# Kernel tuning notes

Measured on AMD Instinct MI355X. Metric: run time of the kernel, lower is better.

## Reference

```python
import jax, jax.numpy as jnp
import numpy as np

N = 50000
E = 800000
IN_DIM = 128
HID = 32
HEADS = 8
OUT_DIM = 2
NEG_SLOPE = 0.2


def setup_inputs() -> dict:
    key = jax.random.key(0)
    ks = jax.random.split(key, 10)
    x = jax.random.normal(ks[0], (N, IN_DIM), dtype=jnp.float32)
    edge_index = jax.random.randint(ks[1], (2, E), 0, N, dtype=jnp.int64)
    s = 0.1
    W1 = jax.random.normal(ks[2], (IN_DIM, HEADS * HID), dtype=jnp.float32) * s
    att_src1 = jax.random.normal(ks[3], (HEADS, HID), dtype=jnp.float32) * s
    att_dst1 = jax.random.normal(ks[4], (HEADS, HID), dtype=jnp.float32) * s
    b1 = jnp.zeros((HEADS * HID,), dtype=jnp.float32)
    W2 = jax.random.normal(ks[5], (HEADS * HID, OUT_DIM), dtype=jnp.float32) * s
    att_src2 = jax.random.normal(ks[6], (1, OUT_DIM), dtype=jnp.float32) * s
    att_dst2 = jax.random.normal(ks[7], (1, OUT_DIM), dtype=jnp.float32) * s
    b2 = jnp.zeros((OUT_DIM,), dtype=jnp.float32)
    return {"x": x, "edge_index": edge_index, "W1": W1, "att_src1": att_src1,
            "att_dst1": att_dst1, "b1": b1, "W2": W2, "att_src2": att_src2,
            "att_dst2": att_dst2, "b2": b2}


def gat_conv(x, src, dst, W, att_src, att_dst, bias, concat):
    # PyG GATConv (add_self_loops handled by caller already appended in src/dst)
    H, C = att_src.shape
    n = x.shape[0]
    h = (x @ W).reshape(n, H, C)                       # [N,H,C]
    a_src = jnp.einsum('nhc,hc->nh', h, att_src)       # [N,H]
    a_dst = jnp.einsum('nhc,hc->nh', h, att_dst)       # [N,H]
    e = jax.nn.leaky_relu(a_src[src] + a_dst[dst], NEG_SLOPE)  # [Etot,H]
    m = jax.lax.stop_gradient(jax.ops.segment_max(e, dst, num_segments=n))
    ee = jnp.exp(e - m[dst])
    denom = jax.ops.segment_sum(ee, dst, num_segments=n)
    alpha = ee / denom[dst]                            # segment softmax over incoming edges
    out = jax.ops.segment_sum(alpha[:, :, None] * h[src], dst, num_segments=n)  # [N,H,C]
    if concat:
        out = out.reshape(n, H * C)
    else:
        out = out.mean(axis=1)
    return out + bias


def reference(x, edge_index, W1, att_src1, att_dst1, b1, W2, att_src2, att_dst2, b2):
    n = x.shape[0]
    loop = jnp.arange(n, dtype=edge_index.dtype)
    src = jnp.concatenate([edge_index[0], loop])
    dst = jnp.concatenate([edge_index[1], loop])
    h = gat_conv(x, src, dst, W1, att_src1, att_dst1, b1, concat=True)
    h = jax.nn.elu(h)
    # dropout inactive in eval mode
    h = gat_conv(h, src, dst, W2, att_src2, att_dst2, b2, concat=False)
    return jax.nn.log_softmax(h, axis=1)
```

## Files before the change

kernel.cpp:

```cpp
#include <hip/hip_runtime.h>
#include <hip/hip_bf16.h>

#define NEG_SLOPE 0.2f
#define BSTRIDE 6144

typedef float f32x4 __attribute__((ext_vector_type(4)));
typedef short s16x4 __attribute__((ext_vector_type(4)));
typedef short bf16x8 __attribute__((ext_vector_type(8)));

__device__ __forceinline__ float lrelu(float x) { return x > 0.f ? x : NEG_SLOPE * x; }
__device__ __forceinline__ float bf2f(unsigned u) {
    return __uint_as_float(u << 16);
}
__device__ __forceinline__ unsigned short f2bf(float f) {
    unsigned int u = __float_as_uint(f);
    return (unsigned short)((u + 0x7FFF + ((u >> 16) & 1)) >> 16);
}

__global__ __launch_bounds__(256) void prep_kernel(
        const float* __restrict__ W1, const float* __restrict__ att_src1,
        const float* __restrict__ att_dst1, unsigned short* __restrict__ w1t,
        const int* __restrict__ ei, int* __restrict__ flag, int* __restrict__ bktCur) {
    int t = threadIdx.x;
    if (blockIdx.x < 128) {
        int v = blockIdx.x * 256 + t;
        int col = v & 255, k = v >> 8;
        w1t[(size_t)col * 128 + k] = f2bf(W1[(size_t)k * 256 + col]);
    } else if (blockIdx.x == 128) {
#pragma unroll
        for (int i = 0; i < 8; ++i) {
            int v = t + 256 * i;
            int j = v & 15, k = v >> 4;
            const float* av = (j < 8) ? att_src1 : att_dst1;
            int h = j & 7;
            float s = 0.f;
            for (int c = 0; c < 32; ++c)
                s += W1[(size_t)k * 256 + 32 * h + c] * av[h * 32 + c];
            w1t[(size_t)(256 + j) * 128 + k] = f2bf(s);
        }
    } else {
        bktCur[t] = t * BSTRIDE;
        if (t == 0) {
            int z = 1;
            for (int k = 0; k < 64; ++k) if (ei[2 * k + 1] != 0) { z = 0; break; }
            *flag = z;
        }
    }
}

__global__ __launch_bounds__(256) void bin_scatter(const int* __restrict__ ei, int E, int n,
                                                   const int* __restrict__ flag,
                                                   int* __restrict__ bktCur,
                                                   int* __restrict__ binned) {
    __shared__ int hist[256];
    __shared__ int gb[256];
    int t = threadIdx.x;
    hist[t] = 0;
    __syncthreads();
    int is64 = *flag;
    int base = blockIdx.x * 2048;
    int Etot = E + n;
    int rec[8], rb[8], rr[8];
#pragma unroll
    for (int k = 0; k < 8; ++k) {
        int e = base + k * 256 + t;
        rb[k] = -1;
        if (e < Etot) {
            int s, d;
            if (e < E) {
                if (is64) {
                    s = ((const int2*)ei)[e].x;
                    d = ((const int2*)(ei + 2 * (size_t)E))[e].x;
                } else {
                    s = ei[e];
                    d = ei[(size_t)E + e];
                }
            } else { s = d = e - E; }
            int b = d >> 8;
            rb[k] = b;
            rec[k] = s | ((d & 255) << 24);
            rr[k] = atomicAdd(&hist[b], 1);
        }
    }
    __syncthreads();
    if (hist[t]) gb[t] = atomicAdd(&bktCur[t], hist[t]);
    __syncthreads();
#pragma unroll
    for (int k = 0; k < 8; ++k)
        if (rb[k] >= 0) binned[gb[rb[k]] + rr[k]] = rec[k];
}

__device__ __forceinline__ bf16x8 read_frag(const char* base, int row, int kb) {
    int swz = (row & 7) << 4;
    const char* p = base + row * 256;
    s16x4 lo = *(const s16x4*)(p + (kb ^ swz));
    s16x4 hi = *(const s16x4*)(p + ((kb + 32) ^ swz));
    return __builtin_shufflevector(lo, hi, 0, 1, 2, 3, 4, 5, 6, 7);
}

__device__ __forceinline__ void load_px(const float* __restrict__ x, int m0, int n, int t,
                                        f32x4 (&px)[2][4]) {
#pragma unroll
    for (int q = 0; q < 2; ++q) {
        int u = t + 256 * q;
        int row = u >> 3, kseg = u & 7;
        int gr = m0 + row;
        bool ok = (u < 384) && (gr < n);
        const f32x4* p = (const f32x4*)(x + (size_t)gr * 128 + kseg * 16);
#pragma unroll
        for (int j = 0; j < 4; ++j) {
            f32x4 z = {0.f, 0.f, 0.f, 0.f};
            px[q][j] = ok ? p[j] : z;
        }
    }
}

#define XOFF 69632
__global__ __launch_bounds__(256, 2) void build_gemm_kernel(
        const int* __restrict__ bktCur, const int* __restrict__ binned,
        int* __restrict__ offs, int* __restrict__ degOut, int* __restrict__ csr,
        const float* __restrict__ x, const unsigned short* __restrict__ w1t,
        unsigned short* __restrict__ h1u, float* __restrict__ asrc1,
        float* __restrict__ adst1, int n, int nchunk, int ngemm) {
    __shared__ __align__(16) char lds[81920];
    const int t = threadIdx.x;

    if (blockIdx.x >= ngemm) {
        int* deg = (int*)lds;
        int* sd  = (int*)(lds + 1024);
        int b = blockIdx.x - ngemm;
        int lo = b * BSTRIDE, hi = bktCur[b];
        deg[t] = 0;
        __syncthreads();
        for (int i = lo + t; i < hi; i += 256)
            atomicAdd(&deg[((unsigned)binned[i]) >> 24], 1);
        __syncthreads();
        int v = deg[t];
        sd[t] = v;
        __syncthreads();
        for (int o = 1; o < 256; o <<= 1) {
            int xv = (t >= o) ? sd[t - o] : 0;
            __syncthreads();
            sd[t] += xv;
            __syncthreads();
        }
        int excl = lo + sd[t] - v;
        int node = (b << 8) + t;
        if (node < n) { offs[node] = excl; degOut[node] = v; }
        __syncthreads();
        deg[t] = excl;
        __syncthreads();
        for (int i = lo + t; i < hi; i += 256) {
            unsigned r = (unsigned)binned[i];
            int pos = atomicAdd(&deg[r >> 24], 1);
            csr[pos] = (int)(r & 0xFFFFFF);
        }
        return;
    }

    const int lane = t & 63, w = t >> 6;
    const int l15 = lane & 15, g = lane >> 4;

    for (int u = t; u < 4352; u += 256) {
        int col = u >> 4, seg = u & 15;
        int4 v = *(const int4*)(w1t + (size_t)col * 128 + seg * 8);
        *(int4*)(lds + col * 256 + ((seg * 16) ^ ((col & 7) << 4))) = v;
    }

    int c0 = blockIdx.x * 2;
    f32x4 px[2][4];
    load_px(x, c0 * 48, n, t, px);
    __syncthreads();

    bf16x8 Bf[4][5];
#pragma unroll
    for (int ks = 0; ks < 4; ++ks) {
#pragma unroll
        for (int nt = 0; nt < 5; ++nt) {
            if (nt < 4 || w == 0) {
                int col = (nt < 4) ? (64 * w + 16 * nt + l15) : (256 + l15);
                Bf[ks][nt] = read_frag(lds, col, 64 * ks + 8 * g);
            }
        }
    }

    for (int cc = 0; cc < 2; ++cc) {
        int chunk = c0 + cc;
        if (chunk >= nchunk) break;
        int m0 = chunk * 48;
#pragma unroll
        for (int q = 0; q < 2; ++q) {
            int u = t + 256 * q;
            if (u < 384) {
                int row = u >> 3, kseg = u & 7;
                union { unsigned short us[16]; int4 v[2]; } pk;
#pragma unroll
                for (int j = 0; j < 4; ++j)
#pragma unroll
                    for (int e = 0; e < 4; ++e) pk.us[j * 4 + e] = f2bf(px[q][j][e]);
                int base = XOFF + row * 256;
                int swz = (row & 7) << 4;
                *(int4*)(lds + base + ((kseg * 32) ^ swz)) = pk.v[0];
                *(int4*)(lds + base + ((kseg * 32 + 16) ^ swz)) = pk.v[1];
            }
        }
        __syncthreads();
        if (cc == 0) load_px(x, (c0 + 1) * 48, n, t, px);

        f32x4 acc[3][5];
#pragma unroll
        for (int mt = 0; mt < 3; ++mt)
#pragma unroll
            for (int nt = 0; nt < 5; ++nt)
#pragma unroll
                for (int r = 0; r < 4; ++r) acc[mt][nt][r] = 0.f;

#pragma unroll
        for (int ks = 0; ks < 4; ++ks) {
            bf16x8 Af[3];
#pragma unroll
            for (int mt = 0; mt < 3; ++mt)
                Af[mt] = read_frag(lds + XOFF, mt * 16 + l15, 64 * ks + 8 * g);
#pragma unroll
            for (int nt = 0; nt < 5; ++nt) {
                if (nt < 4 || w == 0) {
#pragma unroll
                    for (int mt = 0; mt < 3; ++mt)
                        acc[mt][nt] = __builtin_amdgcn_mfma_f32_16x16x32_bf16(
                            Af[mt], Bf[ks][nt], acc[mt][nt], 0, 0, 0);
                }
            }
        }

#pragma unroll
        for (int mt = 0; mt < 3; ++mt) {
#pragma unroll
            for (int r = 0; r < 4; ++r) {
                int row = m0 + 16 * mt + 4 * g + r;
                bool ok = row < n;
#pragma unroll
                for (int nt = 0; nt < 4; ++nt)
                    if (ok) h1u[(size_t)row * 256 + 64 * w + 16 * nt + l15] =
                        f2bf(acc[mt][nt][r]);
                if (w == 0 && ok) {
                    float v = acc[mt][4][r];
                    if (l15 < 8) asrc1[(size_t)row * 8 + l15] = v;
                    else         adst1[(size_t)row * 8 + (l15 - 8)] = v;
                }
            }
        }
        if (cc == 0) __syncthreads();
    }
}

__global__ __launch_bounds__(64) void aggregate_kernel(
        const int* __restrict__ offs, const int* __restrict__ deg,
        const int* __restrict__ csr,
        const float* __restrict__ asrc1, const float* __restrict__ adst1,
        const unsigned short* __restrict__ h1u, const float* __restrict__ b1,
        const float* __restrict__ W2, const float* __restrict__ att_src2,
        const float* __restrict__ att_dst2, float4* __restrict__ rec) {
    int d = blockIdx.x;
    int t = threadIdx.x;
    int h = t >> 3;
    int off = offs[d], end = off + deg[d];
    float ad = adst1[(size_t)d * 8 + h];
    float a0 = 0.f, a1 = 0.f, a2 = 0.f, a3 = 0.f, aw = 0.f;
    const unsigned short* hp = h1u + 4 * t;
    int i = off;
    for (; i + 8 <= end; i += 8) {
        int sIdx[8];
#pragma unroll
        for (int k = 0; k < 8; ++k) sIdx[k] = csr[i + k];
        float wv[8];
#pragma unroll
        for (int k = 0; k < 8; ++k)
            wv[k] = __expf(lrelu(asrc1[(size_t)sIdx[k] * 8 + h] + ad));
        ushort4 hv[8];
#pragma unroll
        for (int k = 0; k < 8; ++k)
            hv[k] = *(const ushort4*)(hp + (size_t)sIdx[k] * 256);
#pragma unroll
        for (int k = 0; k < 8; ++k) {
            a0 = fmaf(wv[k], bf2f(hv[k].x), a0);
            a1 = fmaf(wv[k], bf2f(hv[k].y), a1);
            a2 = fmaf(wv[k], bf2f(hv[k].z), a2);
            a3 = fmaf(wv[k], bf2f(hv[k].w), a3);
            aw += wv[k];
        }
    }
    for (; i < end; ++i) {
        int s = csr[i];
        float w = __expf(lrelu(asrc1[(size_t)s * 8 + h] + ad));
        ushort4 v = *(const ushort4*)(hp + (size_t)s * 256);
        a0 = fmaf(w, bf2f(v.x), a0); a1 = fmaf(w, bf2f(v.y), a1);
        a2 = fmaf(w, bf2f(v.z), a2); a3 = fmaf(w, bf2f(v.w), a3);
        aw += w;
    }
    float inv = 1.0f / aw;
    float4 bv = *(const float4*)(b1 + 4 * t);
    float v0 = fmaf(a0, inv, bv.x);
    float v1 = fmaf(a1, inv, bv.y);
    float v2 = fmaf(a2, inv, bv.z);
    float v3 = fmaf(a3, inv, bv.w);
    v0 = v0 > 0.f ? v0 : __expf(v0) - 1.f;
    v1 = v1 > 0.f ? v1 : __expf(v1) - 1.f;
    v2 = v2 > 0.f ? v2 : __expf(v2) - 1.f;
    v3 = v3 > 0.f ? v3 : __expf(v3) - 1.f;
    float4 w01 = *(const float4*)(W2 + 8 * t);
    float4 w23 = *(const float4*)(W2 + 8 * t + 4);
    float p0 = v0 * w01.x + v1 * w01.z + v2 * w23.x + v3 * w23.z;
    float p1 = v0 * w01.y + v1 * w01.w + v2 * w23.y + v3 * w23.w;
#pragma unroll
    for (int o = 32; o; o >>= 1) { p0 += __shfl_down(p0, o); p1 += __shfl_down(p1, o); }
    if (t == 0) {
        float s2a = att_src2[0], s2b = att_src2[1];
        float d2a = att_dst2[0], d2b = att_dst2[1];
        rec[d] = make_float4(p0, p1, p0 * s2a + p1 * s2b, p0 * d2a + p1 * d2b);
    }
}

__global__ __launch_bounds__(256) void layer2_kernel(
        const int* __restrict__ offs, const int* __restrict__ deg,
        const int* __restrict__ csr, const float4* __restrict__ rec,
        const float* __restrict__ b2, float* __restrict__ out, int n) {
    int t = threadIdx.x;
    int d = blockIdx.x * 16 + (t >> 4);
    if (d >= n) return;
    int li = t & 15;
    int off = offs[d], end = off + deg[d];
    float ad = rec[d].w;
    float se = 0.f, s0 = 0.f, s1 = 0.f;
    for (int i = off + li; i < end; i += 16) {
        int s = csr[i];
        float4 r = rec[s];
        float e = __expf(lrelu(r.z + ad));
        se += e;
        s0 = fmaf(e, r.x, s0);
        s1 = fmaf(e, r.y, s1);
    }
#pragma unroll
    for (int o = 8; o; o >>= 1) {
        se += __shfl_xor(se, o, 16);
        s0 += __shfl_xor(s0, o, 16);
        s1 += __shfl_xor(s1, o, 16);
    }
    if (li == 0) {
        float o0 = s0 / se + b2[0];
        float o1 = s1 / se + b2[1];
        float m2 = fmaxf(o0, o1);
        float lse = m2 + logf(__expf(o0 - m2) + __expf(o1 - m2));
        out[(size_t)d * 2 + 0] = o0 - lse;
        out[(size_t)d * 2 + 1] = o1 - lse;
    }
}

extern "C" void kernel_launch(void* const* d_in, const int* in_sizes, int n_in,
                              void* d_out, int out_size, void* d_ws, size_t ws_size,
                              hipStream_t stream) {
    const float* x        = (const float*)d_in[0];
    const int*   ei       = (const int*)d_in[1];
    const float* W1       = (const float*)d_in[2];
    const float* att_src1 = (const float*)d_in[3];
    const float* att_dst1 = (const float*)d_in[4];
    const float* b1       = (const float*)d_in[5];
    const float* W2       = (const float*)d_in[6];
    const float* att_src2 = (const float*)d_in[7];
    const float* att_dst2 = (const float*)d_in[8];
    const float* b2       = (const float*)d_in[9];
    float* out = (float*)d_out;

    int N = in_sizes[0] / 128;
    int E = in_sizes[1] / 2;
    int Etot = E + N;
    int NB = (N + 255) >> 8;
    int nbs = (Etot + 2047) / 2048;
    int nchunk = (N + 47) / 48;
    int ngemm = (nchunk + 1) / 2;
    size_t binsz = (size_t)NB * BSTRIDE;

    char* W = (char*)d_ws;
    size_t o = 0;
    auto alloc = [&](size_t bytes) { size_t r = o; o = (o + bytes + 15) & ~(size_t)15; return r; };
    unsigned short* h1u  = (unsigned short*)(W + alloc((size_t)N * 256 * 2));
    float*  asrc1   = (float*)(W + alloc((size_t)N * 8 * 4));
    float*  adst1   = (float*)(W + alloc((size_t)N * 8 * 4));
    float4* rec     = (float4*)(W + alloc((size_t)N * 16));
    int*    offs    = (int*)(W + alloc((size_t)N * 4));
    int*    deg     = (int*)(W + alloc((size_t)N * 4));
    int*    bktCur  = (int*)(W + alloc(256 * 4));
    int*    flag    = (int*)(W + alloc(16));
    int*    csr     = (int*)(W + alloc(binsz * 4));
    int*    binned  = (int*)(W + alloc(binsz * 4));
    unsigned short* w1t = (unsigned short*)(W + alloc((size_t)272 * 128 * 2));

    prep_kernel<<<130, 256, 0, stream>>>(W1, att_src1, att_dst1, w1t, ei, flag, bktCur);
    bin_scatter<<<nbs, 256, 0, stream>>>(ei, E, N, flag, bktCur, binned);
    build_gemm_kernel<<<ngemm + NB, 256, 0, stream>>>(bktCur, binned, offs, deg, csr,
                                                      x, w1t, h1u, asrc1, adst1,
                                                      N, nchunk, ngemm);
    aggregate_kernel<<<N, 64, 0, stream>>>(offs, deg, csr, asrc1, adst1, h1u, b1, W2,
                                           att_src2, att_dst2, rec);
    layer2_kernel<<<(N + 15) / 16, 256, 0, stream>>>(offs, deg, csr, rec, b2, out, N);
}
```

Before: 151.6 us.

## Merge prep and bin-scatter kernels, process four GEMM chunks per block

Folds the weight-transpose prep work into the edge bin-scatter launch as extra blocks. Bucket cursors become counts zeroed by a memset, and each scatter block computes the int64 flag itself with a ballot. This removes one dependent kernel launch and its serialization. Separately, each GEMM block now processes four 48-row chunks instead of two, amortizing the weight-fragment LDS load over more rows at the cost of fewer GEMM blocks.

```diff
diff --git a/kernel.cpp b/kernel.cpp
--- a/kernel.cpp
+++ b/kernel.cpp
@@ -3,6 +3,7 @@
 
 #define NEG_SLOPE 0.2f
 #define BSTRIDE 6144
+#define NCHK 4
 
 typedef float f32x4 __attribute__((ext_vector_type(4)));
 typedef short s16x4 __attribute__((ext_vector_type(4)));
@@ -17,47 +18,44 @@
     return (unsigned short)((u + 0x7FFF + ((u >> 16) & 1)) >> 16);
 }
 
-__global__ __launch_bounds__(256) void prep_kernel(
+__global__ __launch_bounds__(256) void scatter_prep_kernel(
+        const int* __restrict__ ei, int E, int n,
+        int* __restrict__ bktCnt, int* __restrict__ binned,
         const float* __restrict__ W1, const float* __restrict__ att_src1,
-        const float* __restrict__ att_dst1, unsigned short* __restrict__ w1t,
-        const int* __restrict__ ei, int* __restrict__ flag, int* __restrict__ bktCur) {
+        const float* __restrict__ att_dst1, unsigned short* __restrict__ w1t, int nbs) {
     int t = threadIdx.x;
-    if (blockIdx.x < 128) {
-        int v = blockIdx.x * 256 + t;
-        int col = v & 255, k = v >> 8;
-        w1t[(size_t)col * 128 + k] = f2bf(W1[(size_t)k * 256 + col]);
-    } else if (blockIdx.x == 128) {
-#pragma unroll
-        for (int i = 0; i < 8; ++i) {
-            int v = t + 256 * i;
-            int j = v & 15, k = v >> 4;
-            const float* av = (j < 8) ? att_src1 : att_dst1;
-            int h = j & 7;
-            float s = 0.f;
-            for (int c = 0; c < 32; ++c)
-                s += W1[(size_t)k * 256 + 32 * h + c] * av[h * 32 + c];
-            w1t[(size_t)(256 + j) * 128 + k] = f2bf(s);
-        }
-    } else {
-        bktCur[t] = t * BSTRIDE;
-        if (t == 0) {
-            int z = 1;
-            for (int k = 0; k < 64; ++k) if (ei[2 * k + 1] != 0) { z = 0; break; }
-            *flag = z;
-        }
-    }
-}
-
-__global__ __launch_bounds__(256) void bin_scatter(const int* __restrict__ ei, int E, int n,
-                                                   const int* __restrict__ flag,
-                                                   int* __restrict__ bktCur,
-                                                   int* __restrict__ binned) {
+    if (blockIdx.x >= nbs) {
+        int wb = blockIdx.x - nbs;
+        if (wb < 128) {
+            int v = wb * 256 + t;
+            int col = v & 255, k = v >> 8;
+            w1t[(size_t)col * 128 + k] = f2bf(W1[(size_t)k * 256 + col]);
+        } else {
+#pragma unroll
+            for (int i = 0; i < 8; ++i) {
+                int v = t + 256 * i;
+                int j = v & 15, k = v >> 4;
+                const float* av = (j < 8) ? att_src1 : att_dst1;
+                int h = j & 7;
+                float s = 0.f;
+                for (int c = 0; c < 32; ++c)
+                    s += W1[(size_t)k * 256 + 32 * h + c] * av[h * 32 + c];
+                w1t[(size_t)(256 + j) * 128 + k] = f2bf(s);
+            }
+        }
+        return;
+    }
+
     __shared__ int hist[256];
     __shared__ int gb[256];
-    int t = threadIdx.x;
+    __shared__ int sflag;
     hist[t] = 0;
+    if (t < 64) {
+        unsigned long long m = __ballot(ei[2 * t + 1] != 0);
+        if (t == 0) sflag = (m == 0ULL) ? 1 : 0;
+    }
     __syncthreads();
-    int is64 = *flag;
+    int is64 = sflag;
     int base = blockIdx.x * 2048;
     int Etot = E + n;
     int rec[8], rb[8], rr[8];
@@ -83,7 +81,7 @@
         }
     }
     __syncthreads();
-    if (hist[t]) gb[t] = atomicAdd(&bktCur[t], hist[t]);
+    if (hist[t]) gb[t] = t * BSTRIDE + atomicAdd(&bktCnt[t], hist[t]);
     __syncthreads();
 #pragma unroll
     for (int k = 0; k < 8; ++k)
@@ -117,7 +115,7 @@
 
 #define XOFF 69632
 __global__ __launch_bounds__(256, 2) void build_gemm_kernel(
-        const int* __restrict__ bktCur, const int* __restrict__ binned,
+        const int* __restrict__ bktCnt, const int* __restrict__ binned,
         int* __restrict__ offs, int* __restrict__ degOut, int* __restrict__ csr,
         const float* __restrict__ x, const unsigned short* __restrict__ w1t,
         unsigned short* __restrict__ h1u, float* __restrict__ asrc1,
@@ -129,7 +127,7 @@
         int* deg = (int*)lds;
         int* sd  = (int*)(lds + 1024);
         int b = blockIdx.x - ngemm;
-        int lo = b * BSTRIDE, hi = bktCur[b];
+        int lo = b * BSTRIDE, hi = lo + bktCnt[b];
         deg[t] = 0;
         __syncthreads();
         for (int i = lo + t; i < hi; i += 256)
@@ -167,7 +165,7 @@
         *(int4*)(lds + col * 256 + ((seg * 16) ^ ((col & 7) << 4))) = v;
     }
 
-    int c0 = blockIdx.x * 2;
+    int c0 = blockIdx.x * NCHK;
     f32x4 px[2][4];
     load_px(x, c0 * 48, n, t, px);
     __syncthreads();
@@ -184,7 +182,7 @@
         }
     }
 
-    for (int cc = 0; cc < 2; ++cc) {
+    for (int cc = 0; cc < NCHK; ++cc) {
         int chunk = c0 + cc;
         if (chunk >= nchunk) break;
         int m0 = chunk * 48;
@@ -205,7 +203,7 @@
             }
         }
         __syncthreads();
-        if (cc == 0) load_px(x, (c0 + 1) * 48, n, t, px);
+        if (cc < NCHK - 1) load_px(x, (c0 + cc + 1) * 48, n, t, px);
 
         f32x4 acc[3][5];
 #pragma unroll
@@ -249,7 +247,7 @@
                 }
             }
         }
-        if (cc == 0) __syncthreads();
+        if (cc < NCHK - 1) __syncthreads();
     }
 }
 
@@ -376,7 +374,7 @@
     int NB = (N + 255) >> 8;
     int nbs = (Etot + 2047) / 2048;
     int nchunk = (N + 47) / 48;
-    int ngemm = (nchunk + 1) / 2;
+    int ngemm = (nchunk + NCHK - 1) / NCHK;
     size_t binsz = (size_t)NB * BSTRIDE;
 
     char* W = (char*)d_ws;
@@ -388,15 +386,15 @@
     float4* rec     = (float4*)(W + alloc((size_t)N * 16));
     int*    offs    = (int*)(W + alloc((size_t)N * 4));
     int*    deg     = (int*)(W + alloc((size_t)N * 4));
-    int*    bktCur  = (int*)(W + alloc(256 * 4));
-    int*    flag    = (int*)(W + alloc(16));
+    int*    bktCnt  = (int*)(W + alloc(256 * 4));
     int*    csr     = (int*)(W + alloc(binsz * 4));
     int*    binned  = (int*)(W + alloc(binsz * 4));
     unsigned short* w1t = (unsigned short*)(W + alloc((size_t)272 * 128 * 2));
 
-    prep_kernel<<<130, 256, 0, stream>>>(W1, att_src1, att_dst1, w1t, ei, flag, bktCur);
-    bin_scatter<<<nbs, 256, 0, stream>>>(ei, E, N, flag, bktCur, binned);
-    build_gemm_kernel<<<ngemm + NB, 256, 0, stream>>>(bktCur, binned, offs, deg, csr,
+    hipMemsetAsync(bktCnt, 0, 256 * sizeof(int), stream);
+    scatter_prep_kernel<<<nbs + 129, 256, 0, stream>>>(ei, E, N, bktCnt, binned,
+                                                       W1, att_src1, att_dst1, w1t, nbs);
+    build_gemm_kernel<<<ngemm + NB, 256, 0, stream>>>(bktCnt, binned, offs, deg, csr,
                                                       x, w1t, h1u, asrc1, adst1,
                                                       N, nchunk, ngemm);
     aggregate_kernel<<<N, 64, 0, stream>>>(offs, deg, csr, asrc1, adst1, h1u, b1, W2,
```

After: 141.1 us (median of 2 runs). 6.9% less time.
